# Kernel optimization log

Measured on AMD Instinct MI355X. Metric: run time of the kernel, lower is better.

## Reference

```python
import jax, jax.numpy as jnp
import numpy as np
from jax import lax

B, C, D, H, W = 2, 1, 128, 128, 128
CONSCIOUSNESS_WEIGHT = 0.1


def _field(depth, height, width, dtype):
    # sin(2*pi*(d+h+w)/(D+H+W)) broadcast over batch/channel
    d = jnp.arange(depth, dtype=dtype)[:, None, None]
    h = jnp.arange(height, dtype=dtype)[None, :, None]
    w = jnp.arange(width, dtype=dtype)[None, None, :]
    phase = 2.0 * jnp.pi * (d + h + w) / (depth + height + width)
    return jnp.sin(phase)  # [D,H,W]


def _conv3d(x, w, b):
    y = lax.conv_general_dilated(
        x, w, window_strides=(1, 1, 1), padding='SAME',
        dimension_numbers=('NCDHW', 'OIDHW', 'NCDHW'))
    return y + b[None, :, None, None, None]


def setup_inputs() -> dict:
    key = jax.random.key(0)
    ks = jax.random.split(key, 4)
    fan1 = 1 * 27
    fan2 = 8 * 27
    fan3 = 16 * 27
    return {
        'cube_data': jax.random.normal(ks[0], (B, C, D, H, W), dtype=jnp.float32),
        'w1': jax.random.normal(ks[1], (8, 1, 3, 3, 3), dtype=jnp.float32) / np.sqrt(fan1),
        'b1': jnp.zeros((8,), dtype=jnp.float32),
        'w2': jax.random.normal(ks[2], (16, 8, 3, 3, 3), dtype=jnp.float32) / np.sqrt(fan2),
        'b2': jnp.zeros((16,), dtype=jnp.float32),
        'w3': jax.random.normal(ks[3], (1, 16, 3, 3, 3), dtype=jnp.float32) / np.sqrt(fan3),
        'b3': jnp.zeros((1,), dtype=jnp.float32),
    }


def reference(cube_data, w1, b1, w2, b2, w3, b3):
    _, _, d, h, w = cube_data.shape
    field = _field(d, h, w, cube_data.dtype)[None, None]  # [1,1,D,H,W]
    integrated = cube_data * (1.0 + CONSCIOUSNESS_WEIGHT * field)
    x = jax.nn.relu(_conv3d(integrated, w1, b1))
    x = jax.nn.relu(_conv3d(x, w2, b2))
    x = jnp.tanh(_conv3d(x, w3, b3))
    return x
```

## Files before the change

kernel.cpp:

```cpp
#include <hip/hip_runtime.h>
#include <hip/hip_fp16.h>

#define VOX (128 * 128 * 128)
#define P 130
#define PP (P * P)
#define PVOX (P * P * P)
#define LROW 130
#define NR 18

typedef unsigned short u16;
typedef _Float16 f16x2 __attribute__((ext_vector_type(2)));
typedef _Float16 f16x8 __attribute__((ext_vector_type(8)));
typedef __attribute__((ext_vector_type(4))) float f32x4;
typedef __attribute__((ext_vector_type(2))) float f32x2;

__device__ __forceinline__ u16 f2h(float f) {
    return __builtin_bit_cast(unsigned short, (_Float16)f);
}
__device__ __forceinline__ unsigned pkh_relu(float a, float b) {
    float ra = a > 0.f ? a : 0.f, rb = b > 0.f ? b : 0.f;
    return (unsigned)f2h(ra) | ((unsigned)f2h(rb) << 16);
}
__device__ __forceinline__ f16x2 h2(unsigned u) { return __builtin_bit_cast(f16x2, u); }

__device__ __forceinline__ float dot2(unsigned a, unsigned b, float c) {
#if __has_builtin(__builtin_amdgcn_fdot2)
    return __builtin_amdgcn_fdot2(h2(a), h2(b), c, false);
#else
    f16x2 av = h2(a), bv = h2(b);
    c = fmaf((float)av.x, (float)bv.x, c);
    return fmaf((float)av.y, (float)bv.y, c);
#endif
}

__device__ __forceinline__ float fast_tanh(float x) {
    float e = __expf(2.0f * x);
    return 1.0f - 2.0f * __builtin_amdgcn_rcpf(1.0f + e);
}

__global__ __launch_bounds__(256) void setup_kernel(
    const float* __restrict__ w1, const float* __restrict__ w2,
    const float* __restrict__ w3, u16* __restrict__ w2frag,
    unsigned* __restrict__ w3p, float2* __restrict__ w1p,
    u16* __restrict__ x1, u16* __restrict__ x2) {
    int i = blockIdx.x * 256 + threadIdx.x;
    if (i < 3584) {
        int j = i & 7, l = (i >> 3) & 63, s = i >> 9;
        int tap = s * 4 + (l >> 4), oc = l & 15;
        float v = (tap < 27) ? w2[(oc * 8 + j) * 27 + tap] : 0.0f;
        w2frag[i] = f2h(v);
    }
    if (i < 216) {
        int tap = i >> 3, j = i & 7;
        w3p[i] = (unsigned)f2h(w3[(2 * j) * 27 + tap]) |
                 ((unsigned)f2h(w3[(2 * j + 1) * 27 + tap]) << 16);
    }
    if (i < 108) {
        int tap = i >> 2, j = i & 3;
        w1p[i] = make_float2(w1[(2 * j) * 27 + tap], w1[(2 * j + 1) * 27 + tap]);
    }
    if (i >= PVOX) return;
    int d = i / PP;
    int r = i - d * PP;
    int h = r / P;
    int w = r - h * P;
    if (d == 0 || d == P - 1 || h == 0 || h == P - 1 || w == 0 || w == P - 1) {
        uint4 z = {0u, 0u, 0u, 0u};
        *(uint4*)(x1 + (size_t)i * 8) = z;
        *(uint4*)(x2 + (size_t)i * 16) = z;
        *(uint4*)(x2 + (size_t)i * 16 + 8) = z;
    }
}

__global__ __launch_bounds__(256) void integrate_kernel(
    const float* __restrict__ in, u16* __restrict__ x0) {
    int i = blockIdx.x * 256 + threadIdx.x;
    if (i >= PVOX) return;
    int d = i / PP;
    int r = i - d * PP;
    int h = r / P;
    int w = r - h * P;
    float v = 0.0f;
    if (d >= 1 && d <= 128 && h >= 1 && h <= 128 && w >= 1 && w <= 128) {
        int s = (d - 1) + (h - 1) + (w - 1);
        float fld = 1.0f + 0.1f * sinf(6.283185307179586f * (float)s / 384.0f);
        v = in[(size_t)(d - 1) * 16384 + (h - 1) * 128 + (w - 1)] * fld;
    }
    x0[i] = f2h(v);
}

__global__ __launch_bounds__(256) void conv1_kernel(
    const u16* __restrict__ x0, const float2* __restrict__ w1p,
    const float* __restrict__ b1, u16* __restrict__ x1) {
    const int t = blockIdx.x * 256 + threadIdx.x;
    const int w0 = (t & 63) * 2;
    const int h0 = ((t >> 6) & 31) * 4;
    const int d = t >> 11;

    f32x2 acc[4][4][2];
#pragma unroll
    for (int j = 0; j < 4; ++j) {
        const f32x2 b = {b1[2 * j], b1[2 * j + 1]};
#pragma unroll
        for (int i = 0; i < 4; ++i) { acc[i][j][0] = b; acc[i][j][1] = b; }
    }

#pragma unroll
    for (int dz = 0; dz < 3; ++dz) {
        const u16* zb = x0 + (size_t)(d + dz) * PP + (size_t)h0 * P + w0;
        const float2* wz = w1p + dz * 9 * 4;
#pragma unroll
        for (int r = 0; r < 6; ++r) {
            const u16* rp = zb + r * P;
            const unsigned u0 = *(const unsigned*)rp;
            const unsigned u1 = *(const unsigned*)(rp + 2);
            float vv[4];
            vv[0] = (float)h2(u0).x; vv[1] = (float)h2(u0).y;
            vv[2] = (float)h2(u1).x; vv[3] = (float)h2(u1).y;
#pragma unroll
            for (int dy = 0; dy < 3; ++dy) {
                const int i = r - dy;
                if (i < 0 || i > 3) continue;
#pragma unroll
                for (int dx = 0; dx < 3; ++dx) {
                    const f32x2 s0 = {vv[dx], vv[dx]};
                    const f32x2 s1 = {vv[dx + 1], vv[dx + 1]};
#pragma unroll
                    for (int j = 0; j < 4; ++j) {
                        const float2 wraw = wz[(dy * 3 + dx) * 4 + j];
                        const f32x2 wv = {wraw.x, wraw.y};
                        acc[i][j][0] = __builtin_elementwise_fma(wv, s0, acc[i][j][0]);
                        acc[i][j][1] = __builtin_elementwise_fma(wv, s1, acc[i][j][1]);
                    }
                }
            }
        }
    }
    const size_t e0 = ((size_t)(d + 1) * P + (h0 + 1)) * P + (w0 + 1);
#pragma unroll
    for (int i = 0; i < 4; ++i) {
        uint4 oA, oB;
        oA.x = pkh_relu(acc[i][0][0].x, acc[i][0][0].y);
        oA.y = pkh_relu(acc[i][1][0].x, acc[i][1][0].y);
        oA.z = pkh_relu(acc[i][2][0].x, acc[i][2][0].y);
        oA.w = pkh_relu(acc[i][3][0].x, acc[i][3][0].y);
        oB.x = pkh_relu(acc[i][0][1].x, acc[i][0][1].y);
        oB.y = pkh_relu(acc[i][1][1].x, acc[i][1][1].y);
        oB.z = pkh_relu(acc[i][2][1].x, acc[i][2][1].y);
        oB.w = pkh_relu(acc[i][3][1].x, acc[i][3][1].y);
        *(uint4*)(x1 + (e0 + (size_t)i * P) * 8) = oA;
        *(uint4*)(x1 + (e0 + (size_t)i * P + 1) * 8) = oB;
    }
}

__global__ __launch_bounds__(256) void conv2_mfma_kernel(
    const u16* __restrict__ x1, const u16* __restrict__ w2frag,
    const float* __restrict__ b2, u16* __restrict__ x2) {
    __shared__ u16 sm[NR * LROW * 8];

    const int tid = threadIdx.x;
    const int lane = tid & 63;
    const int wv = tid >> 6;
    const int q = lane >> 4;
    const int mi = lane & 15;
    const int d0 = blockIdx.x >> 5;
    const int h0 = (blockIdx.x & 31) * 4;

    for (int u = tid; u < NR * LROW; u += 256) {
        const int row = u / LROW;
        const int pos = u - row * LROW;
        const int dz = row / 6;
        const int r = row - dz * 6;
        const uint4 v = *(const uint4*)(x1 + ((size_t)((d0 + dz) * P + (h0 + r)) * P + pos) * 8);
        *(uint4*)(sm + (size_t)u * 8) = v;
    }

    f16x8 wf[7];
#pragma unroll
    for (int s = 0; s < 7; ++s)
        wf[s] = *(const f16x8*)(w2frag + (size_t)(s * 64 + lane) * 8);

    __syncthreads();

    f32x4 acc[8];
#pragma unroll
    for (int t = 0; t < 8; ++t) acc[t] = (f32x4){0.f, 0.f, 0.f, 0.f};

#pragma unroll
    for (int s = 0; s < 7; ++s) {
        int tap = s * 4 + q;
        if (tap > 26) tap = 26;
        const int dz = tap / 9;
        const int rem = tap - dz * 9;
        const int dy = rem / 3;
        const int dx = rem - dy * 3;
        const u16* bp = sm + ((dz * 6 + wv + dy) * LROW + (mi + dx)) * 8;
#pragma unroll
        for (int t = 0; t < 8; ++t) {
            f16x8 act = *(const f16x8*)(bp + t * 128);
            acc[t] = __builtin_amdgcn_mfma_f32_16x16x32_f16(wf[s], act, acc[t], 0, 0, 0);
        }
    }

    const float4 bv = *(const float4*)(b2 + q * 4);
    const size_t obase = ((size_t)(d0 + 1) * P + (h0 + wv + 1)) * P + 1;
#pragma unroll
    for (int t = 0; t < 8; ++t) {
        uint2 o;
        o.x = pkh_relu(acc[t][0] + bv.x, acc[t][1] + bv.y);
        o.y = pkh_relu(acc[t][2] + bv.z, acc[t][3] + bv.w);
        *(uint2*)(x2 + (obase + 16 * t + mi) * 16 + q * 4) = o;
    }
}

__global__ __launch_bounds__(256) void conv3_kernel(
    const u16* __restrict__ x2, const unsigned* __restrict__ w3p,
    const float* __restrict__ b3, float* __restrict__ out) {
    const int t = blockIdx.x * 256 + threadIdx.x;
    const int w = t & 127;
    const int h0 = ((t >> 7) & 15) * 8;
    const int d0 = (t >> 11) * 2;

    float accA[2][8], accB[2][8];
#pragma unroll
    for (int dd = 0; dd < 2; ++dd)
#pragma unroll
        for (int i = 0; i < 8; ++i) { accA[dd][i] = 0.f; accB[dd][i] = 0.f; }

#pragma unroll 1
    for (int z = 0; z < 4; ++z) {
        const u16* zb = x2 + ((size_t)((d0 + z) * P + h0) * P + w) * 16;
#pragma unroll
        for (int r = 0; r < 10; ++r) {
            const u16* rp = zb + (size_t)r * (P * 16);
            const uint4 c0l = *(const uint4*)(rp);
            const uint4 c0h = *(const uint4*)(rp + 8);
            const uint4 c1l = *(const uint4*)(rp + 16);
            const uint4 c1h = *(const uint4*)(rp + 24);
            const uint4 c2l = *(const uint4*)(rp + 32);
            const uint4 c2h = *(const uint4*)(rp + 40);
#pragma unroll
            for (int dd = 0; dd < 2; ++dd) {
                const int dz = z - dd;
                if (dz < 0 || dz > 2) continue;
                const unsigned* wz = w3p + dz * 9 * 8;
#pragma unroll
                for (int dy = 0; dy < 3; ++dy) {
                    const int i = r - dy;
                    if (i < 0 || i > 7) continue;
                    const unsigned* wp = wz + dy * 3 * 8;
                    float a = accA[dd][i], b = accB[dd][i];
                    a = dot2(c0l.x, wp[0], a);  b = dot2(c0l.y, wp[1], b);
                    a = dot2(c0l.z, wp[2], a);  b = dot2(c0l.w, wp[3], b);
                    a = dot2(c0h.x, wp[4], a);  b = dot2(c0h.y, wp[5], b);
                    a = dot2(c0h.z, wp[6], a);  b = dot2(c0h.w, wp[7], b);
                    a = dot2(c1l.x, wp[8], a);  b = dot2(c1l.y, wp[9], b);
                    a = dot2(c1l.z, wp[10], a); b = dot2(c1l.w, wp[11], b);
                    a = dot2(c1h.x, wp[12], a); b = dot2(c1h.y, wp[13], b);
                    a = dot2(c1h.z, wp[14], a); b = dot2(c1h.w, wp[15], b);
                    a = dot2(c2l.x, wp[16], a); b = dot2(c2l.y, wp[17], b);
                    a = dot2(c2l.z, wp[18], a); b = dot2(c2l.w, wp[19], b);
                    a = dot2(c2h.x, wp[20], a); b = dot2(c2h.y, wp[21], b);
                    a = dot2(c2h.z, wp[22], a); b = dot2(c2h.w, wp[23], b);
                    accA[dd][i] = a; accB[dd][i] = b;
                }
            }
        }
    }
    const float bias = b3[0];
#pragma unroll
    for (int dd = 0; dd < 2; ++dd) {
        const size_t obase = (size_t)((d0 + dd) * 128 + h0) * 128 + w;
#pragma unroll
        for (int i = 0; i < 8; ++i)
            out[obase + (size_t)i * 128] = fast_tanh(accA[dd][i] + accB[dd][i] + bias);
    }
}

extern "C" void kernel_launch(void* const* d_in, const int* in_sizes, int n_in,
                              void* d_out, int out_size, void* d_ws, size_t ws_size,
                              hipStream_t stream) {
    const float* cube = (const float*)d_in[0];
    const float* w1 = (const float*)d_in[1];
    const float* b1 = (const float*)d_in[2];
    const float* w2 = (const float*)d_in[3];
    const float* b2 = (const float*)d_in[4];
    const float* w3 = (const float*)d_in[5];
    const float* b3 = (const float*)d_in[6];
    float* out = (float*)d_out;

    char* ws = (char*)d_ws;
    u16* w2frag = (u16*)ws;
    unsigned* w3p = (unsigned*)(ws + 7168);
    float2* w1p = (float2*)(ws + 8032);
    u16* x0 = (u16*)(ws + 16384);
    u16* x1 = (u16*)(ws + 16384 + (size_t)PVOX * sizeof(u16));
    u16* x2 = (u16*)(ws + 16384 + (size_t)PVOX * sizeof(u16) + (size_t)PVOX * 8 * sizeof(u16));

    setup_kernel<<<dim3((PVOX + 255) / 256), dim3(256), 0, stream>>>(
        w1, w2, w3, w2frag, w3p, w1p, x1, x2);

    for (int b = 0; b < 2; ++b) {
        integrate_kernel<<<dim3((PVOX + 255) / 256), dim3(256), 0, stream>>>(
            cube + (size_t)b * VOX, x0);
        conv1_kernel<<<dim3(VOX / 8 / 256), dim3(256), 0, stream>>>(x0, w1p, b1, x1);
        conv2_mfma_kernel<<<dim3(128 * 32), dim3(256), 0, stream>>>(x1, w2frag, b2, x2);
        conv3_kernel<<<dim3(VOX / 16 / 256), dim3(256), 0, stream>>>(
            x2, w3p, b3, out + (size_t)b * VOX);
    }
}
```

Baseline: 249.6 us.

## Reuse depth planes in conv2 via rolling LDS ring buffer with register prefetch

```diff
diff --git a/kernel.cpp b/kernel.cpp
--- a/kernel.cpp
+++ b/kernel.cpp
@@ -6,7 +6,7 @@
 #define PP (P * P)
 #define PVOX (P * P * P)
 #define LROW 130
-#define NR 18
+#define PLANE (6 * LROW)
 
 typedef unsigned short u16;
 typedef _Float16 f16x2 __attribute__((ext_vector_type(2)));
@@ -156,60 +156,112 @@
 __global__ __launch_bounds__(256) void conv2_mfma_kernel(
     const u16* __restrict__ x1, const u16* __restrict__ w2frag,
     const float* __restrict__ b2, u16* __restrict__ x2) {
-    __shared__ u16 sm[NR * LROW * 8];
+    __shared__ u16 sm[4 * PLANE * 8];
 
     const int tid = threadIdx.x;
     const int lane = tid & 63;
     const int wv = tid >> 6;
     const int q = lane >> 4;
     const int mi = lane & 15;
-    const int d0 = blockIdx.x >> 5;
+    const int D0 = (blockIdx.x >> 5) * 4;
     const int h0 = (blockIdx.x & 31) * 4;
-
-    for (int u = tid; u < NR * LROW; u += 256) {
-        const int row = u / LROW;
-        const int pos = u - row * LROW;
-        const int dz = row / 6;
-        const int r = row - dz * 6;
-        const uint4 v = *(const uint4*)(x1 + ((size_t)((d0 + dz) * P + (h0 + r)) * P + pos) * 8);
-        *(uint4*)(sm + (size_t)u * 8) = v;
-    }
 
     f16x8 wf[7];
 #pragma unroll
     for (int s = 0; s < 7; ++s)
         wf[s] = *(const f16x8*)(w2frag + (size_t)(s * 64 + lane) * 8);
 
+#pragma unroll 1
+    for (int p = 0; p < 3; ++p) {
+        const int pd = D0 + p;
+        const int slot = pd & 3;
+        for (int u = tid; u < PLANE; u += 256) {
+            const int row = u / LROW;
+            const int pos = u - row * LROW;
+            const uint4 v = *(const uint4*)(x1 + ((size_t)(pd * P + (h0 + row)) * P + pos) * 8);
+            *(uint4*)(sm + ((size_t)(slot * 6 + row) * LROW + pos) * 8) = v;
+        }
+    }
     __syncthreads();
 
-    f32x4 acc[8];
-#pragma unroll
-    for (int t = 0; t < 8; ++t) acc[t] = (f32x4){0.f, 0.f, 0.f, 0.f};
-
-#pragma unroll
-    for (int s = 0; s < 7; ++s) {
-        int tap = s * 4 + q;
-        if (tap > 26) tap = 26;
-        const int dz = tap / 9;
-        const int rem = tap - dz * 9;
-        const int dy = rem / 3;
-        const int dx = rem - dy * 3;
-        const u16* bp = sm + ((dz * 6 + wv + dy) * LROW + (mi + dx)) * 8;
+    const float4 bv = *(const float4*)(b2 + q * 4);
+
+#pragma unroll 1
+    for (int i = 0; i < 4; ++i) {
+        const int dout = D0 + i;
+
+        uint4 pf0, pf1, pf2, pf3;
+        const int pdn = dout + 3;
+        if (i < 3) {
+            {
+                const int u = tid, row = u / LROW, pos = u - row * LROW;
+                pf0 = *(const uint4*)(x1 + ((size_t)(pdn * P + (h0 + row)) * P + pos) * 8);
+            }
+            {
+                const int u = tid + 256, row = u / LROW, pos = u - row * LROW;
+                pf1 = *(const uint4*)(x1 + ((size_t)(pdn * P + (h0 + row)) * P + pos) * 8);
+            }
+            {
+                const int u = tid + 512, row = u / LROW, pos = u - row * LROW;
+                pf2 = *(const uint4*)(x1 + ((size_t)(pdn * P + (h0 + row)) * P + pos) * 8);
+            }
+            if (tid < PLANE - 768) {
+                const int u = tid + 768, row = u / LROW, pos = u - row * LROW;
+                pf3 = *(const uint4*)(x1 + ((size_t)(pdn * P + (h0 + row)) * P + pos) * 8);
+            }
+        }
+
+        f32x4 acc[8];
+#pragma unroll
+        for (int t = 0; t < 8; ++t) acc[t] = (f32x4){0.f, 0.f, 0.f, 0.f};
+
+#pragma unroll
+        for (int s = 0; s < 7; ++s) {
+            int tap = s * 4 + q;
+            if (tap > 26) tap = 26;
+            const int dz = tap / 9;
+            const int rem = tap - dz * 9;
+            const int dy = rem / 3;
+            const int dx = rem - dy * 3;
+            const int slot = (dout + dz) & 3;
+            const u16* bp = sm + ((size_t)(slot * 6 + wv + dy) * LROW + (mi + dx)) * 8;
+#pragma unroll
+            for (int t = 0; t < 8; ++t) {
+                f16x8 act = *(const f16x8*)(bp + t * 128);
+                acc[t] = __builtin_amdgcn_mfma_f32_16x16x32_f16(wf[s], act, acc[t], 0, 0, 0);
+            }
+        }
+
+        const size_t obase = ((size_t)(dout + 1) * P + (h0 + wv + 1)) * P + 1;
 #pragma unroll
         for (int t = 0; t < 8; ++t) {
-            f16x8 act = *(const f16x8*)(bp + t * 128);
-            acc[t] = __builtin_amdgcn_mfma_f32_16x16x32_f16(wf[s], act, acc[t], 0, 0, 0);
-        }
-    }
-
-    const float4 bv = *(const float4*)(b2 + q * 4);
-    const size_t obase = ((size_t)(d0 + 1) * P + (h0 + wv + 1)) * P + 1;
-#pragma unroll
-    for (int t = 0; t < 8; ++t) {
-        uint2 o;
-        o.x = pkh_relu(acc[t][0] + bv.x, acc[t][1] + bv.y);
-        o.y = pkh_relu(acc[t][2] + bv.z, acc[t][3] + bv.w);
-        *(uint2*)(x2 + (obase + 16 * t + mi) * 16 + q * 4) = o;
+            uint2 o;
+            o.x = pkh_relu(acc[t][0] + bv.x, acc[t][1] + bv.y);
+            o.y = pkh_relu(acc[t][2] + bv.z, acc[t][3] + bv.w);
+            *(uint2*)(x2 + (obase + 16 * t + mi) * 16 + q * 4) = o;
+        }
+
+        if (i < 3) {
+            __syncthreads();
+            const int slot = pdn & 3;
+            {
+                const int u = tid, row = u / LROW, pos = u - row * LROW;
+                *(uint4*)(sm + ((size_t)(slot * 6 + row) * LROW + pos) * 8) = pf0;
+            }
+            {
+                const int u = tid + 256, row = u / LROW, pos = u - row * LROW;
+                *(uint4*)(sm + ((size_t)(slot * 6 + row) * LROW + pos) * 8) = pf1;
+            }
+            {
+                const int u = tid + 512, row = u / LROW, pos = u - row * LROW;
+                *(uint4*)(sm + ((size_t)(slot * 6 + row) * LROW + pos) * 8) = pf2;
+            }
+            if (tid < PLANE - 768) {
+                const int u = tid + 768, row = u / LROW, pos = u - row * LROW;
+                *(uint4*)(sm + ((size_t)(slot * 6 + row) * LROW + pos) * 8) = pf3;
+            }
+            __syncthreads();
+        }
     }
 }
 
@@ -304,7 +356,7 @@
         integrate_kernel<<<dim3((PVOX + 255) / 256), dim3(256), 0, stream>>>(
             cube + (size_t)b * VOX, x0);
         conv1_kernel<<<dim3(VOX / 8 / 256), dim3(256), 0, stream>>>(x0, w1p, b1, x1);
-        conv2_mfma_kernel<<<dim3(128 * 32), dim3(256), 0, stream>>>(x1, w2frag, b2, x2);
+        conv2_mfma_kernel<<<dim3(1024), dim3(256), 0, stream>>>(x1, w2frag, b2, x2);
         conv3_kernel<<<dim3(VOX / 16 / 256), dim3(256), 0, stream>>>(
             x2, w3p, b3, out + (size_t)b * VOX);
     }
```

After: 242.8 us. -2.7%, faster.

## Stream depth planes through an LDS ring buffer with async global-to-LDS loads in conv2

Applied to the files above, without the earlier changes.

```diff
diff --git a/kernel.cpp b/kernel.cpp
--- a/kernel.cpp
+++ b/kernel.cpp
@@ -6,7 +6,7 @@
 #define PP (P * P)
 #define PVOX (P * P * P)
 #define LROW 130
-#define NR 18
+#define PLANE (6 * LROW)
 
 typedef unsigned short u16;
 typedef _Float16 f16x2 __attribute__((ext_vector_type(2)));
@@ -36,6 +36,13 @@
 __device__ __forceinline__ float fast_tanh(float x) {
     float e = __expf(2.0f * x);
     return 1.0f - 2.0f * __builtin_amdgcn_rcpf(1.0f + e);
+}
+
+__device__ __forceinline__ void gload_lds16(const u16* g, u16* l) {
+    __builtin_amdgcn_global_load_lds(
+        (const __attribute__((address_space(1))) unsigned int*)g,
+        (__attribute__((address_space(3))) unsigned int*)l,
+        16, 0, 0);
 }
 
 __global__ __launch_bounds__(256) void setup_kernel(
@@ -156,60 +163,88 @@
 __global__ __launch_bounds__(256) void conv2_mfma_kernel(
     const u16* __restrict__ x1, const u16* __restrict__ w2frag,
     const float* __restrict__ b2, u16* __restrict__ x2) {
-    __shared__ u16 sm[NR * LROW * 8];
+    __shared__ u16 sm[4 * PLANE * 8];
 
     const int tid = threadIdx.x;
     const int lane = tid & 63;
     const int wv = tid >> 6;
     const int q = lane >> 4;
     const int mi = lane & 15;
-    const int d0 = blockIdx.x >> 5;
+    const int D0 = (blockIdx.x >> 5) * 4;
     const int h0 = (blockIdx.x & 31) * 4;
-
-    for (int u = tid; u < NR * LROW; u += 256) {
-        const int row = u / LROW;
-        const int pos = u - row * LROW;
-        const int dz = row / 6;
-        const int r = row - dz * 6;
-        const uint4 v = *(const uint4*)(x1 + ((size_t)((d0 + dz) * P + (h0 + r)) * P + pos) * 8);
-        *(uint4*)(sm + (size_t)u * 8) = v;
-    }
 
     f16x8 wf[7];
 #pragma unroll
     for (int s = 0; s < 7; ++s)
         wf[s] = *(const f16x8*)(w2frag + (size_t)(s * 64 + lane) * 8);
 
+#pragma unroll
+    for (int p = 0; p < 3; ++p) {
+        const int pd = D0 + p;
+        const int slot = pd & 3;
+        const u16* gb = x1 + ((size_t)(pd * P + h0) * P) * 8;
+        u16* lb = sm + (size_t)slot * PLANE * 8;
+#pragma unroll
+        for (int k = 0; k < 3; ++k) {
+            const int u0 = wv * 64 + k * 256;
+            gload_lds16(gb + (size_t)(u0 + lane) * 8, lb + (size_t)u0 * 8);
+        }
+        if (wv == 0 && lane < PLANE - 768)
+            gload_lds16(gb + (size_t)(768 + lane) * 8, lb + (size_t)768 * 8);
+    }
     __syncthreads();
 
-    f32x4 acc[8];
-#pragma unroll
-    for (int t = 0; t < 8; ++t) acc[t] = (f32x4){0.f, 0.f, 0.f, 0.f};
-
-#pragma unroll
-    for (int s = 0; s < 7; ++s) {
-        int tap = s * 4 + q;
-        if (tap > 26) tap = 26;
-        const int dz = tap / 9;
-        const int rem = tap - dz * 9;
-        const int dy = rem / 3;
-        const int dx = rem - dy * 3;
-        const u16* bp = sm + ((dz * 6 + wv + dy) * LROW + (mi + dx)) * 8;
+    const float4 bv = *(const float4*)(b2 + q * 4);
+
+#pragma unroll 1
+    for (int i = 0; i < 4; ++i) {
+        const int dout = D0 + i;
+
+        if (i < 3) {
+            const int pd = dout + 3;
+            const int slot = pd & 3;
+            const u16* gb = x1 + ((size_t)(pd * P + h0) * P) * 8;
+            u16* lb = sm + (size_t)slot * PLANE * 8;
+#pragma unroll
+            for (int k = 0; k < 3; ++k) {
+                const int u0 = wv * 64 + k * 256;
+                gload_lds16(gb + (size_t)(u0 + lane) * 8, lb + (size_t)u0 * 8);
+            }
+            if (wv == 0 && lane < PLANE - 768)
+                gload_lds16(gb + (size_t)(768 + lane) * 8, lb + (size_t)768 * 8);
+        }
+
+        f32x4 acc[8];
+#pragma unroll
+        for (int t = 0; t < 8; ++t) acc[t] = (f32x4){0.f, 0.f, 0.f, 0.f};
+
+#pragma unroll
+        for (int s = 0; s < 7; ++s) {
+            int tap = s * 4 + q;
+            if (tap > 26) tap = 26;
+            const int dz = tap / 9;
+            const int rem = tap - dz * 9;
+            const int dy = rem / 3;
+            const int dx = rem - dy * 3;
+            const int slot = (dout + dz) & 3;
+            const u16* bp = sm + ((size_t)(slot * 6 + wv + dy) * LROW + (mi + dx)) * 8;
+#pragma unroll
+            for (int t = 0; t < 8; ++t) {
+                f16x8 act = *(const f16x8*)(bp + t * 128);
+                acc[t] = __builtin_amdgcn_mfma_f32_16x16x32_f16(wf[s], act, acc[t], 0, 0, 0);
+            }
+        }
+
+        const size_t obase = ((size_t)(dout + 1) * P + (h0 + wv + 1)) * P + 1;
 #pragma unroll
         for (int t = 0; t < 8; ++t) {
-            f16x8 act = *(const f16x8*)(bp + t * 128);
-            acc[t] = __builtin_amdgcn_mfma_f32_16x16x32_f16(wf[s], act, acc[t], 0, 0, 0);
-        }
-    }
-
-    const float4 bv = *(const float4*)(b2 + q * 4);
-    const size_t obase = ((size_t)(d0 + 1) * P + (h0 + wv + 1)) * P + 1;
-#pragma unroll
-    for (int t = 0; t < 8; ++t) {
-        uint2 o;
-        o.x = pkh_relu(acc[t][0] + bv.x, acc[t][1] + bv.y);
-        o.y = pkh_relu(acc[t][2] + bv.z, acc[t][3] + bv.w);
-        *(uint2*)(x2 + (obase + 16 * t + mi) * 16 + q * 4) = o;
+            uint2 o;
+            o.x = pkh_relu(acc[t][0] + bv.x, acc[t][1] + bv.y);
+            o.y = pkh_relu(acc[t][2] + bv.z, acc[t][3] + bv.w);
+            *(uint2*)(x2 + (obase + 16 * t + mi) * 16 + q * 4) = o;
+        }
+
+        if (i < 3) __syncthreads();
     }
 }
 
@@ -304,7 +339,7 @@
         integrate_kernel<<<dim3((PVOX + 255) / 256), dim3(256), 0, stream>>>(
             cube + (size_t)b * VOX, x0);
         conv1_kernel<<<dim3(VOX / 8 / 256), dim3(256), 0, stream>>>(x0, w1p, b1, x1);
-        conv2_mfma_kernel<<<dim3(128 * 32), dim3(256), 0, stream>>>(x1, w2frag, b2, x2);
+        conv2_mfma_kernel<<<dim3(1024), dim3(256), 0, stream>>>(x1, w2frag, b2, x2);
         conv3_kernel<<<dim3(VOX / 16 / 256), dim3(256), 0, stream>>>(
             x2, w3p, b3, out + (size_t)b * VOX);
     }
```

Result: faster. 227.7 us (-8.7%).
